# Kernel optimization log

Hardware: AMD Instinct MI355X
Metric: run time of the kernel (lower is better)

The kernel has to match this reference:

```python
import jax, jax.numpy as jnp
import numpy as np

KH = KW = 3
STRIDE = 1
PAD = 1
DIL = 1


def _bilinear_gather(data, py, px):
    # data: [B,C,H,W]; py,px: [B,KK,Ho,Wo] absolute sample coords
    B, C, H, W = data.shape
    y0 = jnp.floor(py)
    x0 = jnp.floor(px)
    wy1 = py - y0  # frac weights
    wx1 = px - x0
    wy0 = 1.0 - wy1
    wx0 = 1.0 - wx1
    flat = data.reshape(B, C, H * W)

    def gather(yi, xi):
        valid = (yi >= 0) & (yi < H) & (xi >= 0) & (xi < W)
        yc = jnp.clip(yi, 0, H - 1).astype(jnp.int32)
        xc = jnp.clip(xi, 0, W - 1).astype(jnp.int32)
        idx = yc * W + xc  # [B,KK,Ho,Wo]
        vals = jax.vmap(lambda im, ix: im[:, ix])(flat, idx)  # [B,C,KK,Ho,Wo]
        return vals * valid[:, None].astype(data.dtype)

    out = (gather(y0, x0) * (wy0 * wx0)[:, None]
           + gather(y0, x0 + 1) * (wy0 * wx1)[:, None]
           + gather(y0 + 1, x0) * (wy1 * wx0)[:, None]
           + gather(y0 + 1, x0 + 1) * (wy1 * wx1)[:, None])
    return out  # [B,C,KK,Ho,Wo]


def setup_inputs() -> dict:
    key = jax.random.key(0)
    k1, k2, k3 = jax.random.split(key, 3)
    data = jax.random.normal(k1, (8, 64, 128, 128), dtype=jnp.float32)
    offset = jax.random.normal(k2, (8, 18, 128, 128), dtype=jnp.float32)
    n = 64 * KH * KW
    stdv = 1.0 / np.sqrt(n)
    weight = jax.random.uniform(k3, (64, 64, KH, KW), dtype=jnp.float32,
                                minval=-stdv, maxval=stdv)
    return {"data": data, "offset": offset, "weight": weight}


def reference(data, offset, weight):
    B, C, H, W = data.shape
    Ho = (H + 2 * PAD - (DIL * (KH - 1) + 1)) // STRIDE + 1
    Wo = (W + 2 * PAD - (DIL * (KW - 1) + 1)) // STRIDE + 1
    KK = KH * KW
    # offset layout (deformable_groups=1): [B, 2*KK, Ho, Wo], interleaved (dy, dx) per kernel pt
    off = offset.reshape(B, KK, 2, Ho, Wo)
    off_y = off[:, :, 0]  # [B,KK,Ho,Wo]
    off_x = off[:, :, 1]
    ki = (jnp.arange(KK) // KW).astype(data.dtype)  # kernel row
    kj = (jnp.arange(KK) % KW).astype(data.dtype)   # kernel col
    base_y = (jnp.arange(Ho, dtype=data.dtype) * STRIDE - PAD)[None, :, None] \
             + (ki * DIL)[:, None, None]            # [KK,Ho,1]
    base_x = (jnp.arange(Wo, dtype=data.dtype) * STRIDE - PAD)[None, None, :] \
             + (kj * DIL)[:, None, None]            # [KK,1,Wo]
    py = off_y + base_y[None]  # [B,KK,Ho,Wo]
    px = off_x + base_x[None]
    sampled = _bilinear_gather(data, py, px)  # [B,C,KK,Ho,Wo]
    O = weight.shape[0]
    out = jnp.einsum('bckhw,ock->bohw', sampled, weight.reshape(O, C, KK))
    return out
```

## Files before the change

### kernel.cpp

```cpp
#include <hip/hip_runtime.h>

#define HH 128
#define WW 128
#define CC 64
#define OO 64
#define KK 9
#define PLANE (HH * WW)
#define BAND 10
#define BAND_BYTES (BAND * 128 * 64)
#define OVF_SLOTS 32
#define OVF_BASE BAND_BYTES

typedef _Float16 half8v __attribute__((ext_vector_type(8)));
typedef _Float16 half2v __attribute__((ext_vector_type(2)));
typedef float floatx4 __attribute__((ext_vector_type(4)));

__device__ __forceinline__ unsigned bf16pack_u(float lo, float hi) {
    unsigned a = __float_as_uint(lo);
    unsigned b = __float_as_uint(hi);
    return ((a + 0x7fffu + ((a >> 16) & 1u)) >> 16) |
           ((b + 0x7fffu + ((b >> 16) & 1u)) & 0xffff0000u);
}
__device__ __forceinline__ unsigned pk2(float x) {
    return __builtin_bit_cast(unsigned, __builtin_amdgcn_cvt_pkrtz(x, x));
}
__device__ __forceinline__ half2v h2(unsigned u) {
    return __builtin_bit_cast(half2v, u);
}

__global__ __launch_bounds__(256)
void nhwc_f16_kernel(const float* __restrict__ in, unsigned short* __restrict__ outT) {
    __shared__ unsigned tile[64 * 36];
    int raw = blockIdx.x;
    int b = raw & 7;
    int rest = raw >> 3;
    int y = rest >> 1;
    int xh = rest & 1;
    int t = threadIdx.x;
    int p = t & 63;
    int cg = t >> 6;
    const float* src = in + (size_t)(b * 64) * PLANE + y * WW + xh * 64 + p;
#pragma unroll
    for (int i = 0; i < 8; ++i) {
        int c0 = cg * 16 + 2 * i;
        float v0 = src[(size_t)c0 * PLANE];
        float v1 = src[(size_t)(c0 + 1) * PLANE];
        unsigned lo = __builtin_bit_cast(unsigned short, (_Float16)v0);
        unsigned hi = __builtin_bit_cast(unsigned short, (_Float16)v1);
        tile[p * 36 + (c0 >> 1)] = lo | (hi << 16);
    }
    __syncthreads();
    int p2 = t >> 2;
    int q = t & 3;
    const unsigned* s = &tile[p2 * 36 + q * 8];
    uint4 w0 = *(const uint4*)s;
    uint4 w1 = *(const uint4*)(s + 4);
    int half = q >> 1;
    char* dst = (char*)outT + ((size_t)(b * 2 + half) << 20)
              + (size_t)(y * 128 + xh * 64 + p2) * 64 + (q & 1) * 32;
    *(uint4*)dst = w0;
    *(uint4*)(dst + 16) = w1;
}

__global__ void wprep_kernel(const float* __restrict__ w, _Float16* __restrict__ wt4) {
    int idx = blockIdx.x * 256 + threadIdx.x;
    if (idx < 2 * KK * 4 * 64 * 8) {
        int j = idx & 7;
        int lane = (idx >> 3) & 63;
        int nt = (idx >> 9) & 3;
        int pk = idx >> 11;
        int k = pk % 9;
        int pass = pk / 9;
        int o = nt * 16 + (lane & 15);
        int c = pass * 32 + (lane >> 4) * 8 + j;
        wt4[idx] = (_Float16)w[(o * 64 + c) * 9 + k];
    }
}

__global__ __launch_bounds__(256, 1)
void deform_mfma_kernel(const unsigned short* __restrict__ dataT,
                        const float* __restrict__ offset,
                        const _Float16* __restrict__ wt4,
                        float* __restrict__ out) {
    __shared__ uint4 bandBuf4[(BAND_BYTES + OVF_SLOTS * 128) / 16];
    __shared__ uint2 dOff[KK][128];
    __shared__ uint4 dW[KK][128];
    __shared__ unsigned ovfSrc[OVF_SLOTS];
    __shared__ int ovfCnt;

    const int t = threadIdx.x;
    const int lane = t & 63;
    const int w = t >> 6;
    const int quad = lane >> 4;
    const int l15 = lane & 15;
    const int raw = blockIdx.x;
    const int b = raw & 7;
    const int ho = raw >> 3;
    const int mbase = w * 32;
    const int bs = min(max(ho - 4, 0), HH - BAND);

    if (t == 0) ovfCnt = 0;
    __syncthreads();

#pragma unroll
    for (int i = 0; i < 5; ++i) {
        int u = i * 256 + t;
        if (u < KK * 128) {
            int px = u & 127;
            int k = u >> 7;
            const float* offp = offset + ((size_t)(b * 18) + 2 * k) * PLANE + ho * WW + px;
            float oy = offp[0];
            float ox = offp[PLANE];
            float py = (float)(ho - 1 + k / 3) + oy;
            float pxx = (float)(px - 1 + k % 3) + ox;
            float y0f = floorf(py);
            float x0f = floorf(pxx);
            float fy = py - y0f;
            float fx = pxx - x0f;
            int y0 = (int)y0f, x0 = (int)x0f;
            int y1 = y0 + 1, x1 = x0 + 1;
            float wy0 = (1.f - fy) * ((y0 >= 0 && y0 < HH) ? 1.f : 0.f);
            float wy1 = fy * ((y1 >= 0 && y1 < HH) ? 1.f : 0.f);
            float wx0 = (1.f - fx) * ((x0 >= 0 && x0 < WW) ? 1.f : 0.f);
            float wx1 = fx * ((x1 >= 0 && x1 < WW) ? 1.f : 0.f);
            int yc0 = min(max(y0, 0), HH - 1);
            int yc1 = min(max(y1, 0), HH - 1);
            int x_lo = min(max(x0, 0), WW - 2);
            float wA = ((x0 == x_lo) ? wx0 : 0.f) + ((x1 == x_lo) ? wx1 : 0.f);
            float wB = ((x0 == x_lo + 1) ? wx0 : 0.f) + ((x1 == x_lo + 1) ? wx1 : 0.f);

            unsigned off0, off1;
            {
                int r0 = yc0 - bs;
                if (wy0 == 0.f) off0 = (unsigned)(x_lo * 64);
                else if ((unsigned)r0 < BAND) off0 = (unsigned)((r0 * 128 + x_lo) * 64);
                else {
                    int slot = atomicAdd(&ovfCnt, 1);
                    if (slot < OVF_SLOTS) {
                        ovfSrc[slot] = (unsigned)((yc0 * 128 + x_lo) * 64);
                        off0 = (unsigned)(OVF_BASE + slot * 128);
                    } else {
                        int rc = min(max(r0, 0), BAND - 1);
                        off0 = (unsigned)((rc * 128 + x_lo) * 64);
                    }
                }
            }
            {
                int r1 = yc1 - bs;
                if (wy1 == 0.f) off1 = (unsigned)(x_lo * 64);
                else if ((unsigned)r1 < BAND) off1 = (unsigned)((r1 * 128 + x_lo) * 64);
                else {
                    int slot = atomicAdd(&ovfCnt, 1);
                    if (slot < OVF_SLOTS) {
                        ovfSrc[slot] = (unsigned)((yc1 * 128 + x_lo) * 64);
                        off1 = (unsigned)(OVF_BASE + slot * 128);
                    } else {
                        int rc = min(max(r1, 0), BAND - 1);
                        off1 = (unsigned)((rc * 128 + x_lo) * 64);
                    }
                }
            }
            dOff[k][px] = make_uint2(off0, off1);
            dW[k][px] = make_uint4(pk2(wy0 * wA), pk2(wy0 * wB),
                                   pk2(wy1 * wA), pk2(wy1 * wB));
        }
    }
    __syncthreads();
    const int cnt = min(ovfCnt, OVF_SLOTS);

    floatx4 acc[2][4];
#pragma unroll
    for (int mt = 0; mt < 2; ++mt)
#pragma unroll
        for (int nt = 0; nt < 4; ++nt)
            acc[mt][nt] = (floatx4){0.f, 0.f, 0.f, 0.f};

    const unsigned qoff = (unsigned)(quad * 16);
    char* bb = (char*)bandBuf4;

    for (int pass = 0; pass < 2; ++pass) {
        {
            const char* gsrc = (const char*)dataT + ((size_t)(b * 2 + pass) << 20)
                             + (unsigned)(bs * 8192);
#pragma unroll
            for (int i = 0; i < 20; ++i) {
                int u = i * 256 + t;
                uint4 v = *(const uint4*)(gsrc + (size_t)u * 16);
                *(uint4*)(bb + u * 16) = v;
            }
            if (t < cnt * 8) {
                int s = t >> 3, j = t & 7;
                const char* g2 = (const char*)dataT + ((size_t)(b * 2 + pass) << 20)
                               + ovfSrc[s] + j * 16;
                uint4 v = *(const uint4*)g2;
                *(uint4*)(bb + OVF_BASE + t * 16) = v;
            }
        }
        __syncthreads();

        for (int k = 0; k < KK; ++k) {
            uint4 bfr[4];
            const uint4* wk = (const uint4*)wt4 + (size_t)((pass * 9 + k) * 4) * 64 + lane;
#pragma unroll
            for (int nt = 0; nt < 4; ++nt) bfr[nt] = wk[nt * 64];

#pragma unroll
            for (int mt = 0; mt < 2; ++mt) {
                int px = mbase + mt * 16 + l15;
                uint2 doff = dOff[k][px];
                uint4 ww = dW[k][px];
                half2v h00 = h2(ww.x), h01 = h2(ww.y), h10 = h2(ww.z), h11 = h2(ww.w);
                uint4 v00 = *(const uint4*)(bb + doff.x + qoff);
                uint4 v01 = *(const uint4*)(bb + doff.x + 64 + qoff);
                uint4 v10 = *(const uint4*)(bb + doff.y + qoff);
                uint4 v11 = *(const uint4*)(bb + doff.y + 64 + qoff);
                half2v s0 = h2(v00.x) * h00 + h2(v01.x) * h01 + h2(v10.x) * h10 + h2(v11.x) * h11;
                half2v s1 = h2(v00.y) * h00 + h2(v01.y) * h01 + h2(v10.y) * h10 + h2(v11.y) * h11;
                half2v s2 = h2(v00.z) * h00 + h2(v01.z) * h01 + h2(v10.z) * h10 + h2(v11.z) * h11;
                half2v s3 = h2(v00.w) * h00 + h2(v01.w) * h01 + h2(v10.w) * h10 + h2(v11.w) * h11;
                uint4 sv = make_uint4(__builtin_bit_cast(unsigned, s0),
                                      __builtin_bit_cast(unsigned, s1),
                                      __builtin_bit_cast(unsigned, s2),
                                      __builtin_bit_cast(unsigned, s3));
                half8v afrag = __builtin_bit_cast(half8v, sv);
#pragma unroll
                for (int nt = 0; nt < 4; ++nt)
                    acc[mt][nt] = __builtin_amdgcn_mfma_f32_16x16x32_f16(
                        afrag, __builtin_bit_cast(half8v, bfr[nt]), acc[mt][nt], 0, 0, 0);
            }
        }
        __syncthreads();
    }

#pragma unroll
    for (int mt = 0; mt < 2; ++mt)
#pragma unroll
        for (int nt = 0; nt < 4; ++nt) {
            int o = nt * 16 + l15;
            int px = mbase + mt * 16 + quad * 4;
            float* dst = out + (size_t)(b * 64 + o) * PLANE + ho * 128 + px;
            *(floatx4*)dst = acc[mt][nt];
        }
}

__global__ void transpose_weight_kernel(const float* __restrict__ w,
                                        float* __restrict__ wt) {
    int i = blockIdx.x * 256 + threadIdx.x;
    if (i < CC * KK * OO) {
        int o = i & 63;
        int ck = i >> 6;
        wt[i] = w[o * (CC * KK) + ck];
    }
}

__global__ __launch_bounds__(256)
void deform_conv_kernel(const float* __restrict__ data,
                        const float* __restrict__ offset,
                        const float* __restrict__ wt,
                        float* __restrict__ out) {
    const int tid = threadIdx.x;
    const int wo = tid & 127;
    int ohalf = tid >> 7;
    ohalf = __builtin_amdgcn_readfirstlane(ohalf);
    const int row = blockIdx.x;
    const int b = row >> 7;
    const int ho = row & 127;
    int abyte[KK][4];
    float wgt[KK][4];
    const float* offBase = offset + ((size_t)b * 18) * PLANE + ho * WW + wo;
#pragma unroll
    for (int k = 0; k < KK; ++k) {
        float oy = offBase[(2 * k) * PLANE];
        float ox = offBase[(2 * k + 1) * PLANE];
        float py = oy + (float)(ho - 1 + k / 3);
        float px = ox + (float)(wo - 1 + k % 3);
        float y0f = floorf(py);
        float x0f = floorf(px);
        float wy1 = py - y0f, wx1 = px - x0f;
        float wy0 = 1.f - wy1, wx0 = 1.f - wx1;
        int y0 = (int)y0f, x0 = (int)x0f;
        int y1 = y0 + 1, x1 = x0 + 1;
        float my0 = (y0 >= 0 && y0 < HH) ? 1.f : 0.f;
        float my1 = (y1 >= 0 && y1 < HH) ? 1.f : 0.f;
        float mx0 = (x0 >= 0 && x0 < WW) ? 1.f : 0.f;
        float mx1 = (x1 >= 0 && x1 < WW) ? 1.f : 0.f;
        int yc0 = min(max(y0, 0), HH - 1);
        int yc1 = min(max(y1, 0), HH - 1);
        int xc0 = min(max(x0, 0), WW - 1);
        int xc1 = min(max(x1, 0), WW - 1);
        abyte[k][0] = (yc0 * WW + xc0) * 4;
        abyte[k][1] = (yc0 * WW + xc1) * 4;
        abyte[k][2] = (yc1 * WW + xc0) * 4;
        abyte[k][3] = (yc1 * WW + xc1) * 4;
        wgt[k][0] = wy0 * wx0 * my0 * mx0;
        wgt[k][1] = wy0 * wx1 * my0 * mx1;
        wgt[k][2] = wy1 * wx0 * my1 * mx0;
        wgt[k][3] = wy1 * wx1 * my1 * mx1;
    }
    float acc[32];
#pragma unroll
    for (int j = 0; j < 32; ++j) acc[j] = 0.f;
    const float* planeBase = data + (size_t)b * CC * PLANE;
    const float4* wt4base = (const float4*)wt + ohalf * 8;
    for (int c = 0; c < CC; ++c) {
        const char* pc = (const char*)(planeBase + c * PLANE);
#pragma unroll
        for (int k = 0; k < KK; ++k) {
            float v00 = *(const float*)(pc + abyte[k][0]);
            float v01 = *(const float*)(pc + abyte[k][1]);
            float v10 = *(const float*)(pc + abyte[k][2]);
            float v11 = *(const float*)(pc + abyte[k][3]);
            float s = wgt[k][0] * v00 + wgt[k][1] * v01 +
                      wgt[k][2] * v10 + wgt[k][3] * v11;
            const float4* wp = wt4base + (c * KK + k) * 16;
#pragma unroll
            for (int j = 0; j < 8; ++j) {
                float4 wv = wp[j];
                acc[4 * j + 0] += s * wv.x;
                acc[4 * j + 1] += s * wv.y;
                acc[4 * j + 2] += s * wv.z;
                acc[4 * j + 3] += s * wv.w;
            }
        }
    }
    float* outp = out + ((size_t)b * OO + ohalf * 32) * PLANE + ho * WW + wo;
#pragma unroll
    for (int j = 0; j < 32; ++j) outp[j * PLANE] = acc[j];
}

extern "C" void kernel_launch(void* const* d_in, const int* in_sizes, int n_in,
                              void* d_out, int out_size, void* d_ws, size_t ws_size,
                              hipStream_t stream) {
    const float* data = (const float*)d_in[0];
    const float* offset = (const float*)d_in[1];
    const float* weight = (const float*)d_in[2];
    float* out = (float*)d_out;

    const size_t DATA_T_BYTES = (size_t)8 * 2 * 128 * 128 * 64;
    const size_t WT4_BYTES = (size_t)2 * KK * 4 * 64 * 8 * 2;

    if (ws_size >= DATA_T_BYTES + WT4_BYTES) {
        unsigned short* dataT = (unsigned short*)d_ws;
        _Float16* wt4 = (_Float16*)((char*)d_ws + DATA_T_BYTES);
        nhwc_f16_kernel<<<8 * 128 * 2, 256, 0, stream>>>(data, dataT);
        wprep_kernel<<<(2 * KK * 4 * 64 * 8 + 255) / 256, 256, 0, stream>>>(weight, wt4);
        deform_mfma_kernel<<<8 * HH, 256, 0, stream>>>(dataT, offset, wt4, out);
    } else {
        float* wt = (float*)d_ws;
        int nw = CC * KK * OO;
        transpose_weight_kernel<<<(nw + 255) / 256, 256, 0, stream>>>(weight, wt);
        deform_conv_kernel<<<8 * HH, 256, 0, stream>>>(data, offset, wt, out);
    }
}
```

Baseline: 142.2 us.

## Process two output rows per block with padded LDS band and packed descriptors

```diff
diff --git a/kernel.cpp b/kernel.cpp
--- a/kernel.cpp
+++ b/kernel.cpp
@@ -6,86 +6,84 @@
 #define OO 64
 #define KK 9
 #define PLANE (HH * WW)
-#define BAND 10
-#define BAND_BYTES (BAND * 128 * 64)
-#define OVF_SLOTS 32
-#define OVF_BASE BAND_BYTES
+
+#define BAND 11
+#define PXB 72
+#define BAND_B (BAND * 128 * PXB)
+#define POOL_SLOTS 64
+#define POOL_OFF BAND_B
+#define POOL_B (POOL_SLOTS * 144)
+#define DESC_OFF (POOL_OFF + POOL_B)
+#define LDS_TOTAL (DESC_OFF + KK * 256 * 16)
 
 typedef _Float16 half8v __attribute__((ext_vector_type(8)));
 typedef _Float16 half2v __attribute__((ext_vector_type(2)));
 typedef float floatx4 __attribute__((ext_vector_type(4)));
 
-__device__ __forceinline__ unsigned bf16pack_u(float lo, float hi) {
-    unsigned a = __float_as_uint(lo);
-    unsigned b = __float_as_uint(hi);
-    return ((a + 0x7fffu + ((a >> 16) & 1u)) >> 16) |
-           ((b + 0x7fffu + ((b >> 16) & 1u)) & 0xffff0000u);
-}
-__device__ __forceinline__ unsigned pk2(float x) {
-    return __builtin_bit_cast(unsigned, __builtin_amdgcn_cvt_pkrtz(x, x));
+__device__ __forceinline__ unsigned pkpair(float a, float b) {
+    return __builtin_bit_cast(unsigned, __builtin_amdgcn_cvt_pkrtz(a, b));
 }
 __device__ __forceinline__ half2v h2(unsigned u) {
     return __builtin_bit_cast(half2v, u);
 }
 
 __global__ __launch_bounds__(256)
-void nhwc_f16_kernel(const float* __restrict__ in, unsigned short* __restrict__ outT) {
+void prep_kernel(const float* __restrict__ in, const float* __restrict__ wsrc,
+                 unsigned short* __restrict__ outT, _Float16* __restrict__ wt4) {
     __shared__ unsigned tile[64 * 36];
-    int raw = blockIdx.x;
-    int b = raw & 7;
-    int rest = raw >> 3;
-    int y = rest >> 1;
-    int xh = rest & 1;
+    int blk = blockIdx.x;
     int t = threadIdx.x;
-    int p = t & 63;
-    int cg = t >> 6;
-    const float* src = in + (size_t)(b * 64) * PLANE + y * WW + xh * 64 + p;
-#pragma unroll
-    for (int i = 0; i < 8; ++i) {
-        int c0 = cg * 16 + 2 * i;
-        float v0 = src[(size_t)c0 * PLANE];
-        float v1 = src[(size_t)(c0 + 1) * PLANE];
-        unsigned lo = __builtin_bit_cast(unsigned short, (_Float16)v0);
-        unsigned hi = __builtin_bit_cast(unsigned short, (_Float16)v1);
-        tile[p * 36 + (c0 >> 1)] = lo | (hi << 16);
-    }
-    __syncthreads();
-    int p2 = t >> 2;
-    int q = t & 3;
-    const unsigned* s = &tile[p2 * 36 + q * 8];
-    uint4 w0 = *(const uint4*)s;
-    uint4 w1 = *(const uint4*)(s + 4);
-    int half = q >> 1;
-    char* dst = (char*)outT + ((size_t)(b * 2 + half) << 20)
-              + (size_t)(y * 128 + xh * 64 + p2) * 64 + (q & 1) * 32;
-    *(uint4*)dst = w0;
-    *(uint4*)(dst + 16) = w1;
-}
-
-__global__ void wprep_kernel(const float* __restrict__ w, _Float16* __restrict__ wt4) {
-    int idx = blockIdx.x * 256 + threadIdx.x;
-    if (idx < 2 * KK * 4 * 64 * 8) {
-        int j = idx & 7;
-        int lane = (idx >> 3) & 63;
-        int nt = (idx >> 9) & 3;
-        int pk = idx >> 11;
-        int k = pk % 9;
-        int pass = pk / 9;
-        int o = nt * 16 + (lane & 15);
-        int c = pass * 32 + (lane >> 4) * 8 + j;
-        wt4[idx] = (_Float16)w[(o * 64 + c) * 9 + k];
-    }
-}
-
-__global__ __launch_bounds__(256, 1)
+    if (blk < 2048) {
+        int b = blk & 7;
+        int rest = blk >> 3;
+        int y = rest >> 1;
+        int xh = rest & 1;
+        int p = t & 63;
+        int cg = t >> 6;
+        const float* src = in + (size_t)(b * 64) * PLANE + y * WW + xh * 64 + p;
+#pragma unroll
+        for (int i = 0; i < 8; ++i) {
+            int c0 = cg * 16 + 2 * i;
+            float v0 = src[(size_t)c0 * PLANE];
+            float v1 = src[(size_t)(c0 + 1) * PLANE];
+            unsigned lo = __builtin_bit_cast(unsigned short, (_Float16)v0);
+            unsigned hi = __builtin_bit_cast(unsigned short, (_Float16)v1);
+            tile[p * 36 + (c0 >> 1)] = lo | (hi << 16);
+        }
+        __syncthreads();
+        int p2 = t >> 2;
+        int q = t & 3;
+        const unsigned* s = &tile[p2 * 36 + q * 8];
+        uint4 w0 = *(const uint4*)s;
+        uint4 w1 = *(const uint4*)(s + 4);
+        int half = q >> 1;
+        char* dst = (char*)outT + ((size_t)(b * 2 + half) << 20)
+                  + (size_t)(y * 128 + xh * 64 + p2) * 64 + (q & 1) * 32;
+        *(uint4*)dst = w0;
+        *(uint4*)(dst + 16) = w1;
+    } else {
+        int idx = (blk - 2048) * 256 + t;
+        if (idx < 2 * KK * 4 * 64 * 8) {
+            int j = idx & 7;
+            int lane = (idx >> 3) & 63;
+            int nt = (idx >> 9) & 3;
+            int pk = idx >> 11;
+            int k = pk % 9;
+            int pass = pk / 9;
+            int o = nt * 16 + (lane & 15);
+            int c = pass * 32 + (lane >> 4) * 8 + j;
+            wt4[idx] = (_Float16)wsrc[(o * 64 + c) * 9 + k];
+        }
+    }
+}
+
+__global__ __launch_bounds__(512, 2)
 void deform_mfma_kernel(const unsigned short* __restrict__ dataT,
                         const float* __restrict__ offset,
                         const _Float16* __restrict__ wt4,
                         float* __restrict__ out) {
-    __shared__ uint4 bandBuf4[(BAND_BYTES + OVF_SLOTS * 128) / 16];
-    __shared__ uint2 dOff[KK][128];
-    __shared__ uint4 dW[KK][128];
-    __shared__ unsigned ovfSrc[OVF_SLOTS];
+    __shared__ __align__(16) char SB[LDS_TOTAL];
+    __shared__ unsigned ovfSrc[POOL_SLOTS];
     __shared__ int ovfCnt;
 
     const int t = threadIdx.x;
@@ -95,24 +93,25 @@
     const int l15 = lane & 15;
     const int raw = blockIdx.x;
     const int b = raw & 7;
-    const int ho = raw >> 3;
-    const int mbase = w * 32;
-    const int bs = min(max(ho - 4, 0), HH - BAND);
+    const int ho0 = (raw >> 3) * 2;
+    const int bs = min(max(ho0 - 4, 0), HH - BAND);
 
     if (t == 0) ovfCnt = 0;
     __syncthreads();
 
 #pragma unroll
     for (int i = 0; i < 5; ++i) {
-        int u = i * 256 + t;
-        if (u < KK * 128) {
-            int px = u & 127;
-            int k = u >> 7;
-            const float* offp = offset + ((size_t)(b * 18) + 2 * k) * PLANE + ho * WW + px;
+        int u = i * 512 + t;
+        if (u < KK * 256) {
+            int p = u & 255;
+            int k = u >> 8;
+            int x = p & 127;
+            int ho = ho0 + (p >> 7);
+            const float* offp = offset + ((size_t)(b * 18) + 2 * k) * PLANE + ho * WW + x;
             float oy = offp[0];
             float ox = offp[PLANE];
             float py = (float)(ho - 1 + k / 3) + oy;
-            float pxx = (float)(px - 1 + k % 3) + ox;
+            float pxx = (float)(x - 1 + k % 3) + ox;
             float y0f = floorf(py);
             float x0f = floorf(pxx);
             float fy = py - y0f;
@@ -131,42 +130,45 @@
 
             unsigned off0, off1;
             {
-                int r0 = yc0 - bs;
-                if (wy0 == 0.f) off0 = (unsigned)(x_lo * 64);
-                else if ((unsigned)r0 < BAND) off0 = (unsigned)((r0 * 128 + x_lo) * 64);
+                int r = yc0 - bs;
+                if (wy0 == 0.f) off0 = (unsigned)(x_lo * PXB);
+                else if ((unsigned)r < BAND) off0 = (unsigned)((r * 128 + x_lo) * PXB);
                 else {
                     int slot = atomicAdd(&ovfCnt, 1);
-                    if (slot < OVF_SLOTS) {
+                    if (slot < POOL_SLOTS) {
                         ovfSrc[slot] = (unsigned)((yc0 * 128 + x_lo) * 64);
-                        off0 = (unsigned)(OVF_BASE + slot * 128);
+                        off0 = (unsigned)(POOL_OFF + slot * 144);
                     } else {
-                        int rc = min(max(r0, 0), BAND - 1);
-                        off0 = (unsigned)((rc * 128 + x_lo) * 64);
+                        int rc = min(max(r, 0), BAND - 1);
+                        off0 = (unsigned)((rc * 128 + x_lo) * PXB);
                     }
                 }
             }
             {
-                int r1 = yc1 - bs;
-                if (wy1 == 0.f) off1 = (unsigned)(x_lo * 64);
-                else if ((unsigned)r1 < BAND) off1 = (unsigned)((r1 * 128 + x_lo) * 64);
+                int r = yc1 - bs;
+                if (wy1 == 0.f) off1 = (unsigned)(x_lo * PXB);
+                else if ((unsigned)r < BAND) off1 = (unsigned)((r * 128 + x_lo) * PXB);
                 else {
                     int slot = atomicAdd(&ovfCnt, 1);
-                    if (slot < OVF_SLOTS) {
+                    if (slot < POOL_SLOTS) {
                         ovfSrc[slot] = (unsigned)((yc1 * 128 + x_lo) * 64);
-                        off1 = (unsigned)(OVF_BASE + slot * 128);
+                        off1 = (unsigned)(POOL_OFF + slot * 144);
                     } else {
-                        int rc = min(max(r1, 0), BAND - 1);
-                        off1 = (unsigned)((rc * 128 + x_lo) * 64);
+                        int rc = min(max(r, 0), BAND - 1);
+                        off1 = (unsigned)((rc * 128 + x_lo) * PXB);
                     }
                 }
             }
-            dOff[k][px] = make_uint2(off0, off1);
-            dW[k][px] = make_uint4(pk2(wy0 * wA), pk2(wy0 * wB),
-                                   pk2(wy1 * wA), pk2(wy1 * wB));
+            uint4 d;
+            d.x = (off0 >> 3) | ((off1 >> 3) << 16);
+            d.y = pkpair(wy0 * wA, wy0 * wB);
+            d.z = pkpair(wy1 * wA, wy1 * wB);
+            d.w = 0;
+            *(uint4*)(SB + DESC_OFF + (size_t)(k * 256 + p) * 16) = d;
         }
     }
     __syncthreads();
-    const int cnt = min(ovfCnt, OVF_SLOTS);
+    const int cnt = min(ovfCnt, POOL_SLOTS);
 
     floatx4 acc[2][4];
 #pragma unroll
@@ -176,24 +178,23 @@
             acc[mt][nt] = (floatx4){0.f, 0.f, 0.f, 0.f};
 
     const unsigned qoff = (unsigned)(quad * 16);
-    char* bb = (char*)bandBuf4;
 
     for (int pass = 0; pass < 2; ++pass) {
+        if (pass) __syncthreads();
+        const char* gh = (const char*)dataT + ((size_t)(b * 2 + pass) << 20);
         {
-            const char* gsrc = (const char*)dataT + ((size_t)(b * 2 + pass) << 20)
-                             + (unsigned)(bs * 8192);
-#pragma unroll
-            for (int i = 0; i < 20; ++i) {
-                int u = i * 256 + t;
+            const char* gsrc = gh + (unsigned)(bs * 8192);
+#pragma unroll
+            for (int i = 0; i < 11; ++i) {
+                int u = i * 512 + t;
                 uint4 v = *(const uint4*)(gsrc + (size_t)u * 16);
-                *(uint4*)(bb + u * 16) = v;
+                int pxl = u >> 2, q = u & 3;
+                *(uint4*)(SB + pxl * PXB + q * 16) = v;
             }
             if (t < cnt * 8) {
-                int s = t >> 3, j = t & 7;
-                const char* g2 = (const char*)dataT + ((size_t)(b * 2 + pass) << 20)
-                               + ovfSrc[s] + j * 16;
-                uint4 v = *(const uint4*)g2;
-                *(uint4*)(bb + OVF_BASE + t * 16) = v;
+                int s = t >> 3, j = t & 7, ps = j >> 2, q = j & 3;
+                uint4 v = *(const uint4*)(gh + ovfSrc[s] + ps * 64 + q * 16);
+                *(uint4*)(SB + POOL_OFF + s * 144 + ps * 72 + q * 16) = v;
             }
         }
         __syncthreads();
@@ -206,14 +207,19 @@
 
 #pragma unroll
             for (int mt = 0; mt < 2; ++mt) {
-                int px = mbase + mt * 16 + l15;
-                uint2 doff = dOff[k][px];
-                uint4 ww = dW[k][px];
-                half2v h00 = h2(ww.x), h01 = h2(ww.y), h10 = h2(ww.z), h11 = h2(ww.w);
-                uint4 v00 = *(const uint4*)(bb + doff.x + qoff);
-                uint4 v01 = *(const uint4*)(bb + doff.x + 64 + qoff);
-                uint4 v10 = *(const uint4*)(bb + doff.y + qoff);
-                uint4 v11 = *(const uint4*)(bb + doff.y + 64 + qoff);
+                int p = w * 32 + mt * 16 + l15;
+                uint4 d = *(const uint4*)(SB + DESC_OFF + (size_t)(k * 256 + p) * 16);
+                unsigned off0 = (d.x & 0xffffu) << 3;
+                unsigned off1 = (d.x >> 16) << 3;
+                half2v wv0 = h2(d.y), wv1 = h2(d.z);
+                half2v h00 = __builtin_shufflevector(wv0, wv0, 0, 0);
+                half2v h01 = __builtin_shufflevector(wv0, wv0, 1, 1);
+                half2v h10 = __builtin_shufflevector(wv1, wv1, 0, 0);
+                half2v h11 = __builtin_shufflevector(wv1, wv1, 1, 1);
+                uint4 v00 = *(const uint4*)(SB + off0 + qoff);
+                uint4 v01 = *(const uint4*)(SB + off0 + 72 + qoff);
+                uint4 v10 = *(const uint4*)(SB + off1 + qoff);
+                uint4 v11 = *(const uint4*)(SB + off1 + 72 + qoff);
                 half2v s0 = h2(v00.x) * h00 + h2(v01.x) * h01 + h2(v10.x) * h10 + h2(v11.x) * h11;
                 half2v s1 = h2(v00.y) * h00 + h2(v01.y) * h01 + h2(v10.y) * h10 + h2(v11.y) * h11;
                 half2v s2 = h2(v00.z) * h00 + h2(v01.z) * h01 + h2(v10.z) * h10 + h2(v11.z) * h11;
@@ -229,7 +235,6 @@
                         afrag, __builtin_bit_cast(half8v, bfr[nt]), acc[mt][nt], 0, 0, 0);
             }
         }
-        __syncthreads();
     }
 
 #pragma unroll
@@ -237,8 +242,10 @@
 #pragma unroll
         for (int nt = 0; nt < 4; ++nt) {
             int o = nt * 16 + l15;
-            int px = mbase + mt * 16 + quad * 4;
-            float* dst = out + (size_t)(b * 64 + o) * PLANE + ho * 128 + px;
+            int p = w * 32 + mt * 16 + quad * 4;
+            int ho = ho0 + (p >> 7);
+            int x = p & 127;
+            float* dst = out + (size_t)(b * 64 + o) * PLANE + ho * 128 + x;
             *(floatx4*)dst = acc[mt][nt];
         }
 }
@@ -342,9 +349,8 @@
     if (ws_size >= DATA_T_BYTES + WT4_BYTES) {
         unsigned short* dataT = (unsigned short*)d_ws;
         _Float16* wt4 = (_Float16*)((char*)d_ws + DATA_T_BYTES);
-        nhwc_f16_kernel<<<8 * 128 * 2, 256, 0, stream>>>(data, dataT);
-        wprep_kernel<<<(2 * KK * 4 * 64 * 8 + 255) / 256, 256, 0, stream>>>(weight, wt4);
-        deform_mfma_kernel<<<8 * HH, 256, 0, stream>>>(dataT, offset, wt4, out);
+        prep_kernel<<<2048 + 144, 256, 0, stream>>>(data, weight, dataT, wt4);
+        deform_mfma_kernel<<<8 * (HH / 2), 512, 0, stream>>>(dataT, offset, wt4, out);
     } else {
         float* wt = (float*)d_ws;
         int nw = CC * KK * OO;
```

After: 130.5 us. 8.3% less time.
